# Kernel optimization log

Hardware: AMD Instinct MI355X
Metric: run time of the kernel (lower is better)

The kernel has to match this reference:

```python
import jax, jax.numpy as jnp
import numpy as np

IN_FEATURES = 4096
OUT_FEATURES = 4096
WBITS = 4
GROUPSIZE = 128
PACK_FACTOR = 32 // WBITS  # 8
MASK = (1 << WBITS) - 1    # 15


def setup_inputs() -> dict:
    key = jax.random.key(0)
    k1, k2, k3, k4, k5 = jax.random.split(key, 5)
    x = jax.random.normal(k1, (4, 2048, IN_FEATURES), dtype=jnp.float32)
    # Packed 4-bit weights: (in_features*wbits//32, out_features) int32 words.
    qweight = jax.random.randint(k2, (IN_FEATURES * WBITS // 32, OUT_FEATURES),
                                 jnp.iinfo(jnp.int32).min, jnp.iinfo(jnp.int32).max,
                                 dtype=jnp.int32)
    num_groups = IN_FEATURES // GROUPSIZE  # 32
    # Packed zero points: (num_groups, out_features*wbits//32) int32 words.
    qzeros = jax.random.randint(k3, (num_groups, OUT_FEATURES * WBITS // 32),
                                jnp.iinfo(jnp.int32).min, jnp.iinfo(jnp.int32).max,
                                dtype=jnp.int32)
    scales = jax.random.uniform(k4, (num_groups, OUT_FEATURES), dtype=jnp.float32,
                                minval=0.001, maxval=0.02)
    bias = jax.random.normal(k5, (OUT_FEATURES,), dtype=jnp.float32)
    return {"x": x, "qweight": qweight, "qzeros": qzeros, "scales": scales, "bias": bias}


def _unpack4(packed, axis_len):
    """Unpack int32 words along a new inner axis of PACK_FACTOR 4-bit nibbles.

    packed: (..., n_words) -> (..., n_words*PACK_FACTOR) int32 in [0, 15].
    """
    shifts = (jnp.arange(PACK_FACTOR, dtype=jnp.int32) * WBITS)
    nib = (packed[..., :, None] >> shifts) & MASK  # (..., n_words, PACK_FACTOR)
    return nib.reshape(*packed.shape[:-1], axis_len)


def reference(x, qweight, qzeros, scales, bias):
    # Unpack weights: qweight is packed along in_features (dim 0).
    # (in/8, 8, out) -> (in, out) int nibbles.
    shifts = (jnp.arange(PACK_FACTOR, dtype=jnp.int32) * WBITS)
    wq = ((qweight[:, None, :] >> shifts[None, :, None]) & MASK)
    wq = wq.reshape(IN_FEATURES, OUT_FEATURES)  # [in, out] int32 in [0,15]
    # Unpack zeros: packed along out_features (dim 1); AutoGPTQ stores zero-1,
    # so add 1 back at dequant time.
    zq = _unpack4(qzeros, OUT_FEATURES) + 1  # [num_groups, out]
    g_idx = jnp.arange(IN_FEATURES, dtype=jnp.int32) // GROUPSIZE  # [in]
    # Per-group affine dequant: W[i,o] = s[g(i),o] * (wq[i,o] - z[g(i),o])
    W = scales[g_idx] * (wq - zq[g_idx]).astype(scales.dtype)  # [in, out]
    # y = x @ W + b  (x: [b, s, in])
    return jnp.einsum('bsi,io->bso', x, W) + bias
```

## Files before the change

### kernel.cpp

```cpp
#include <hip/hip_runtime.h>
#include <hip/hip_bf16.h>
#include <stdint.h>


#define M_TOT 8192
#define N_TOT 4096
#define K_TOT 4096
#define NT    (K_TOT / 64)

using bf16x8 = __attribute__((ext_vector_type(8))) __bf16;
using f32x4  = __attribute__((ext_vector_type(4))) float;

__device__ __forceinline__ unsigned short f2bf(float f) {
  unsigned u = __builtin_bit_cast(unsigned, f);
  u += 0x7fffu + ((u >> 16) & 1u);
  return (unsigned short)(u >> 16);
}

__global__ void cvt_x_kernel(const float* __restrict__ x,
                             unsigned short* __restrict__ xb, int n) {
  int stride = gridDim.x * blockDim.x * 8;
  for (int i = (blockIdx.x * blockDim.x + threadIdx.x) * 8; i < n; i += stride) {
    float4 a = *reinterpret_cast<const float4*>(x + i);
    float4 b = *reinterpret_cast<const float4*>(x + i + 4);
    unsigned short o[8] = {f2bf(a.x), f2bf(a.y), f2bf(a.z), f2bf(a.w),
                           f2bf(b.x), f2bf(b.y), f2bf(b.z), f2bf(b.w)};
    *reinterpret_cast<uint4*>(xb + i) = *reinterpret_cast<const uint4*>(o);
  }
}

__global__ void dequant_wt_kernel(const int* __restrict__ qweight,
                                  const int* __restrict__ qzeros,
                                  const float* __restrict__ scales,
                                  unsigned short* __restrict__ wt) {
  int t = blockIdx.x * blockDim.x + threadIdx.x;
  int nn = t >> 9;
  int kw = t & 511;
  int g  = kw >> 4;
  unsigned w = (unsigned)qweight[kw * N_TOT + nn];
  float s = scales[g * N_TOT + nn];
  unsigned zw = (unsigned)qzeros[g * (N_TOT / 8) + (nn >> 3)];
  float z = (float)(((zw >> ((nn & 7) * 4)) & 15u) + 1u);
  unsigned short o[8];
#pragma unroll
  for (int j = 0; j < 8; ++j) {
    float v = s * ((float)((w >> (4 * j)) & 15u) - z);
    o[j] = f2bf(v);
  }
  *reinterpret_cast<uint4*>(wt + (size_t)nn * K_TOT + kw * 8) =
      *reinterpret_cast<const uint4*>(o);
}

__device__ __forceinline__ void gll16(const unsigned short* g, const unsigned short* l) {
  __builtin_amdgcn_global_load_lds(
      (const __attribute__((address_space(1))) void*)(uintptr_t)g,
      (__attribute__((address_space(3))) void*)(uintptr_t)l, 16, 0, 0);
}

__global__ __launch_bounds__(512, 2) void gemm_8phase_kernel(
    const unsigned short* __restrict__ A,
    const unsigned short* __restrict__ B,
    const float* __restrict__ bias,
    float* __restrict__ C) {
  __shared__ __align__(16) unsigned short As[2 * 256 * 64];
  __shared__ __align__(16) unsigned short Bs[2 * 256 * 64];

  int bid = blockIdx.x;
  int swz = (bid & 7) * 64 + (bid >> 3);
  int bm = swz & 31, bn = swz >> 5;
  int m0 = bm * 256, n0 = bn * 256;

  int t = threadIdx.x;
  int lane = t & 63;
  int wave = t >> 6;
  int wr = wave >> 2, wc = wave & 3;
  int lr = lane & 15, kq = lane >> 4;

  int rowL0 = t >> 3;
  int jlog  = ((t & 7) ^ (rowL0 & 7)) * 8;
  const unsigned short* aG = A + (size_t)(m0 + rowL0) * K_TOT + jlog;
  const unsigned short* bG = B + (size_t)(n0 + rowL0) * K_TOT + jlog;

  unsigned rbA = (unsigned)((wr * 128 + lr) * 128 + ((kq * 16) ^ ((lr & 7) << 4)));
  unsigned rbB = (unsigned)((wc * 64  + lr) * 128 + ((kq * 16) ^ ((lr & 7) << 4)));

  f32x4 acc[8][4] = {};
  bf16x8 av[2][2][2];
  bf16x8 bh[2][4][2];

#define STAGE(matG, ldsArr, tile, h)                                              \
  do {                                                                            \
    const unsigned short* _g = (matG) + (size_t)(h) * 128 * K_TOT +               \
                               (size_t)(tile) * 64;                               \
    const unsigned short* _l = (ldsArr) + ((tile) & 1) * 16384 + (h) * 8192 +     \
                               t * 8;                                             \
    gll16(_g, _l);                                                                \
    gll16(_g + (size_t)64 * K_TOT, _l + 4096);                                    \
  } while (0)

  STAGE(aG, As, 0, 0);
  STAGE(aG, As, 0, 1);
  STAGE(bG, Bs, 0, 0);
  STAGE(bG, Bs, 0, 1);
  STAGE(bG, Bs, 1, 0);
  STAGE(bG, Bs, 1, 1);
  asm volatile("s_waitcnt vmcnt(4)" ::: "memory");
  __builtin_amdgcn_s_barrier();
  __builtin_amdgcn_sched_barrier(0);

  {
    const char* aB0 = (const char*)As;
    const char* bB0 = (const char*)Bs;
#pragma unroll
    for (int n = 0; n < 4; ++n)
#pragma unroll
      for (int s = 0; s < 2; ++s)
        bh[0][n][s] = *(const bf16x8*)(bB0 + ((rbB + n * 2048) ^ (s * 64)));
#pragma unroll
    for (int mm = 0; mm < 2; ++mm)
#pragma unroll
      for (int s = 0; s < 2; ++s)
        av[0][mm][s] = *(const bf16x8*)(aB0 + ((rbA + mm * 2048) ^ (s * 64)));
  }

#pragma unroll 2
  for (int tt = 0; tt < NT; ++tt) {
    const char* aBuf = (const char*)As + (tt & 1) * 32768;

#pragma unroll
    for (int q = 0; q < 4; ++q) {
      __builtin_amdgcn_s_setprio(1);
#pragma unroll
      for (int s = 0; s < 2; ++s)
#pragma unroll
        for (int mm = 0; mm < 2; ++mm)
#pragma unroll
          for (int n = 0; n < 4; ++n)
            acc[2 * q + mm][n] = __builtin_amdgcn_mfma_f32_16x16x32_bf16(
                av[q & 1][mm][s], bh[tt & 1][n][s], acc[2 * q + mm][n], 0, 0, 0);
      __builtin_amdgcn_s_setprio(0);

      if (q < 3) {
#pragma unroll
        for (int mm = 0; mm < 2; ++mm)
#pragma unroll
          for (int s = 0; s < 2; ++s)
            av[(q + 1) & 1][mm][s] = *(const bf16x8*)(
                aBuf + ((rbA + (2 * (q + 1) + mm) * 2048) ^ (s * 64)));
      }

      if (q == 0 && tt + 1 < NT) STAGE(aG, As, tt + 1, 0);
      if (q == 1 && tt + 1 < NT) STAGE(aG, As, tt + 1, 1);
      if (q == 2 && tt + 2 < NT) STAGE(bG, Bs, tt + 2, 0);
      if (q == 3) {
        if (tt + 2 < NT) STAGE(bG, Bs, tt + 2, 1);
        if (tt >= NT - 2) asm volatile("s_waitcnt vmcnt(0)" ::: "memory");
        else              asm volatile("s_waitcnt vmcnt(4)" ::: "memory");
      }

      if (q == 1 || q == 3) __builtin_amdgcn_s_barrier();

      if (q == 3) {
        __builtin_amdgcn_sched_barrier(0);
        if (tt + 1 < NT) {
          const char* aN = (const char*)As + ((tt + 1) & 1) * 32768;
          const char* bN = (const char*)Bs + ((tt + 1) & 1) * 32768;
#pragma unroll
          for (int n = 0; n < 4; ++n)
#pragma unroll
            for (int s = 0; s < 2; ++s)
              bh[(tt + 1) & 1][n][s] =
                  *(const bf16x8*)(bN + ((rbB + n * 2048) ^ (s * 64)));
#pragma unroll
          for (int mm = 0; mm < 2; ++mm)
#pragma unroll
            for (int s = 0; s < 2; ++s)
              av[0][mm][s] = *(const bf16x8*)(aN + ((rbA + mm * 2048) ^ (s * 64)));
        }
      }
    }
  }
#undef STAGE

#pragma unroll
  for (int n = 0; n < 4; ++n) {
    int ncol = n0 + wc * 64 + n * 16 + lr;
    float bz = bias[ncol];
#pragma unroll
    for (int m = 0; m < 8; ++m) {
      int mrow = m0 + wr * 128 + m * 16 + kq * 4;
#pragma unroll
      for (int r = 0; r < 4; ++r)
        C[(size_t)(mrow + r) * N_TOT + ncol] = acc[m][n][r] + bz;
    }
  }
}

extern "C" void kernel_launch(void* const* d_in, const int* in_sizes, int n_in,
                              void* d_out, int out_size, void* d_ws, size_t ws_size,
                              hipStream_t stream) {
  const float* x       = (const float*)d_in[0];
  const int*   qweight = (const int*)d_in[1];
  const int*   qzeros  = (const int*)d_in[2];
  const float* scales  = (const float*)d_in[3];
  const float* bias    = (const float*)d_in[4];
  float* out = (float*)d_out;

  const size_t xb_bytes = (size_t)M_TOT * K_TOT * 2;
  const size_t wt_bytes = (size_t)N_TOT * K_TOT * 2;
  if (ws_size < xb_bytes + wt_bytes) return;

  unsigned short* Xb = (unsigned short*)d_ws;
  unsigned short* Wt = (unsigned short*)((char*)d_ws + xb_bytes);

  cvt_x_kernel<<<2048, 256, 0, stream>>>(x, Xb, M_TOT * K_TOT);
  dequant_wt_kernel<<<(N_TOT * 512) / 256, 256, 0, stream>>>(qweight, qzeros, scales, Wt);

  dim3 grid((M_TOT / 256) * (N_TOT / 256));
  gemm_8phase_kernel<<<grid, 512, 0, stream>>>(Xb, Wt, bias, out);
}
```

Measured before the change: 281.0 us.

## Load B operand directly from global into registers, dropping B LDS staging

```diff
diff --git a/kernel.cpp b/kernel.cpp
--- a/kernel.cpp
+++ b/kernel.cpp
@@ -57,13 +57,12 @@
       (__attribute__((address_space(3))) void*)(uintptr_t)l, 16, 0, 0);
 }
 
-__global__ __launch_bounds__(512, 2) void gemm_8phase_kernel(
+__global__ __launch_bounds__(512, 2) void gemm_breg_kernel(
     const unsigned short* __restrict__ A,
     const unsigned short* __restrict__ B,
     const float* __restrict__ bias,
     float* __restrict__ C) {
   __shared__ __align__(16) unsigned short As[2 * 256 * 64];
-  __shared__ __align__(16) unsigned short Bs[2 * 256 * 64];
 
   int bid = blockIdx.x;
   int swz = (bid & 7) * 64 + (bid >> 3);
@@ -79,49 +78,46 @@
   int rowL0 = t >> 3;
   int jlog  = ((t & 7) ^ (rowL0 & 7)) * 8;
   const unsigned short* aG = A + (size_t)(m0 + rowL0) * K_TOT + jlog;
-  const unsigned short* bG = B + (size_t)(n0 + rowL0) * K_TOT + jlog;
 
   unsigned rbA = (unsigned)((wr * 128 + lr) * 128 + ((kq * 16) ^ ((lr & 7) << 4)));
-  unsigned rbB = (unsigned)((wc * 64  + lr) * 128 + ((kq * 16) ^ ((lr & 7) << 4)));
+
+  const unsigned short* bRow = B + (size_t)(n0 + wc * 64 + lr) * K_TOT + kq * 8;
 
   f32x4 acc[8][4] = {};
   bf16x8 av[2][2][2];
   bf16x8 bh[2][4][2];
 
-#define STAGE(matG, ldsArr, tile, h)                                              \
+#define ASTAGE(tile, h)                                                           \
   do {                                                                            \
-    const unsigned short* _g = (matG) + (size_t)(h) * 128 * K_TOT +               \
+    const unsigned short* _g = aG + (size_t)(h) * 128 * K_TOT +                   \
                                (size_t)(tile) * 64;                               \
-    const unsigned short* _l = (ldsArr) + ((tile) & 1) * 16384 + (h) * 8192 +     \
-                               t * 8;                                             \
+    const unsigned short* _l = As + ((tile) & 1) * 16384 + (h) * 8192 + t * 8;    \
     gll16(_g, _l);                                                                \
     gll16(_g + (size_t)64 * K_TOT, _l + 4096);                                    \
   } while (0)
 
-  STAGE(aG, As, 0, 0);
-  STAGE(aG, As, 0, 1);
-  STAGE(bG, Bs, 0, 0);
-  STAGE(bG, Bs, 0, 1);
-  STAGE(bG, Bs, 1, 0);
-  STAGE(bG, Bs, 1, 1);
-  asm volatile("s_waitcnt vmcnt(4)" ::: "memory");
+#define BLOAD(par, tile)                                                          \
+  do {                                                                            \
+    _Pragma("unroll")                                                             \
+    for (int _n = 0; _n < 4; ++_n)                                                \
+      _Pragma("unroll")                                                           \
+      for (int _s = 0; _s < 2; ++_s)                                              \
+        bh[par][_n][_s] = *(const bf16x8*)(bRow + (size_t)_n * 16 * K_TOT +       \
+                                           (size_t)(tile) * 64 + _s * 32);        \
+  } while (0)
+
+  ASTAGE(0, 0);
+  ASTAGE(0, 1);
+  BLOAD(0, 0);
+  asm volatile("s_waitcnt vmcnt(0)" ::: "memory");
   __builtin_amdgcn_s_barrier();
   __builtin_amdgcn_sched_barrier(0);
 
-  {
-    const char* aB0 = (const char*)As;
-    const char* bB0 = (const char*)Bs;
-#pragma unroll
-    for (int n = 0; n < 4; ++n)
-#pragma unroll
-      for (int s = 0; s < 2; ++s)
-        bh[0][n][s] = *(const bf16x8*)(bB0 + ((rbB + n * 2048) ^ (s * 64)));
-#pragma unroll
-    for (int mm = 0; mm < 2; ++mm)
-#pragma unroll
-      for (int s = 0; s < 2; ++s)
-        av[0][mm][s] = *(const bf16x8*)(aB0 + ((rbA + mm * 2048) ^ (s * 64)));
-  }
+#pragma unroll
+  for (int mm = 0; mm < 2; ++mm)
+#pragma unroll
+    for (int s = 0; s < 2; ++s)
+      av[0][mm][s] = *(const bf16x8*)((const char*)As + ((rbA + mm * 2048) ^ (s * 64)));
 
 #pragma unroll 2
   for (int tt = 0; tt < NT; ++tt) {
@@ -149,28 +145,18 @@
                 aBuf + ((rbA + (2 * (q + 1) + mm) * 2048) ^ (s * 64)));
       }
 
-      if (q == 0 && tt + 1 < NT) STAGE(aG, As, tt + 1, 0);
-      if (q == 1 && tt + 1 < NT) STAGE(aG, As, tt + 1, 1);
-      if (q == 2 && tt + 2 < NT) STAGE(bG, Bs, tt + 2, 0);
+      if (q == 0 && tt + 1 < NT) {
+        BLOAD((tt + 1) & 1, tt + 1);
+        ASTAGE(tt + 1, 0);
+      }
+      if (q == 1 && tt + 1 < NT) ASTAGE(tt + 1, 1);
+
       if (q == 3) {
-        if (tt + 2 < NT) STAGE(bG, Bs, tt + 2, 1);
-        if (tt >= NT - 2) asm volatile("s_waitcnt vmcnt(0)" ::: "memory");
-        else              asm volatile("s_waitcnt vmcnt(4)" ::: "memory");
-      }
-
-      if (q == 1 || q == 3) __builtin_amdgcn_s_barrier();
-
-      if (q == 3) {
+        asm volatile("s_waitcnt vmcnt(0)" ::: "memory");
+        __builtin_amdgcn_s_barrier();
         __builtin_amdgcn_sched_barrier(0);
         if (tt + 1 < NT) {
           const char* aN = (const char*)As + ((tt + 1) & 1) * 32768;
-          const char* bN = (const char*)Bs + ((tt + 1) & 1) * 32768;
-#pragma unroll
-          for (int n = 0; n < 4; ++n)
-#pragma unroll
-            for (int s = 0; s < 2; ++s)
-              bh[(tt + 1) & 1][n][s] =
-                  *(const bf16x8*)(bN + ((rbB + n * 2048) ^ (s * 64)));
 #pragma unroll
           for (int mm = 0; mm < 2; ++mm)
 #pragma unroll
@@ -180,7 +166,8 @@
       }
     }
   }
-#undef STAGE
+#undef ASTAGE
+#undef BLOAD
 
 #pragma unroll
   for (int n = 0; n < 4; ++n) {
@@ -217,5 +204,5 @@
   dequant_wt_kernel<<<(N_TOT * 512) / 256, 256, 0, stream>>>(qweight, qzeros, scales, Wt);
 
   dim3 grid((M_TOT / 256) * (N_TOT / 256));
-  gemm_8phase_kernel<<<grid, 512, 0, stream>>>(Xb, Wt, bias, out);
-}
+  gemm_breg_kernel<<<grid, 512, 0, stream>>>(Xb, Wt, bias, out);
+}
```

Result: slower. 414.6 us (+47.5%).
